# Kernel tuning notes

Measured on AMD Instinct MI355X. Metric: run time of the kernel, lower is better.

The kernel has to match this reference:

```python
import jax, jax.numpy as jnp
import numpy as np
from jax import lax

T = 16        # in_length
E = 32        # input_embedding_size_d
H = 64        # encoder_size
NG = 32       # vehicles per scene group
G = 1024      # number of scene groups
N = G * NG    # total vehicles
C = 3         # class_num

leaky = lambda x: jax.nn.leaky_relu(x, 0.1)

def _gru_final(x_seq, Wih, Whh, bih, bhh):
    # x_seq: (T, N, E). PyTorch GRU gate order: r, z, n. Returns final hidden (N, H).
    def step(h, x):
        gx = x @ Wih.T + bih
        gh = h @ Whh.T + bhh
        xr, xz, xn = jnp.split(gx, 3, axis=-1)
        hr, hz, hn = jnp.split(gh, 3, axis=-1)
        r = jax.nn.sigmoid(xr + hr)
        z = jax.nn.sigmoid(xz + hz)
        ng = jnp.tanh(xn + r * hn)
        return (1.0 - z) * ng + z * h, None
    h0 = jnp.zeros((x_seq.shape[1], Whh.shape[1]), x_seq.dtype)
    hT, _ = lax.scan(step, h0, x_seq)
    return hT

def setup_inputs() -> dict:
    key = jax.random.key(0)
    ks = jax.random.split(key, 24)
    def rn(k, shape, fan):
        return jax.random.normal(k, shape, jnp.float32) * np.float32(1.0 / np.sqrt(fan))
    inp = {}
    inp["scene"] = jax.random.normal(ks[0], (N, 2 * T), jnp.float32)
    inp["condition"] = jax.random.randint(ks[1], (N,), 0, C, jnp.int32)
    inp["hero_pos_index"] = jax.random.randint(ks[2], (G,), 0, N, jnp.int32)
    inp["nbrs_pos_index"] = jax.random.randint(ks[3], (N,), 0, N, jnp.int32)
    inp["index_div"] = jnp.arange(N, dtype=jnp.int32).reshape(G, NG)
    # ip_emb_d: Linear(2, E)
    inp["W_emb"] = rn(ks[4], (2, E), 2)
    inp["b_emb"] = jnp.zeros((E,), jnp.float32)
    # forward / backward GRUs (weight_ih: (3H,E), weight_hh: (3H,H))
    inp["Wih_f"] = rn(ks[5], (3 * H, E), E); inp["Whh_f"] = rn(ks[6], (3 * H, H), H)
    inp["bih_f"] = jnp.zeros((3 * H,), jnp.float32); inp["bhh_f"] = jnp.zeros((3 * H,), jnp.float32)
    inp["Wih_b"] = rn(ks[7], (3 * H, E), E); inp["Whh_b"] = rn(ks[8], (3 * H, H), H)
    inp["bih_b"] = jnp.zeros((3 * H,), jnp.float32); inp["bhh_b"] = jnp.zeros((3 * H,), jnp.float32)
    # mlp: Linear(H, H//2)
    inp["Wm"] = rn(ks[9], (H, H // 2), H); inp["bm"] = jnp.zeros((H // 2,), jnp.float32)
    # spatial_mlp: Linear(2T, H) -> Linear(H, H//2)
    inp["Ws1"] = rn(ks[10], (2 * T, H), 2 * T); inp["bs1"] = jnp.zeros((H,), jnp.float32)
    inp["Ws2"] = rn(ks[11], (H, H // 2), H); inp["bs2"] = jnp.zeros((H // 2,), jnp.float32)
    # op_d: Linear(H, H//4) -> Linear(H//4, C)
    inp["Wo1"] = rn(ks[12], (H, H // 4), H); inp["bo1"] = jnp.zeros((H // 4,), jnp.float32)
    inp["Wo2"] = rn(ks[13], (H // 4, C), H // 4); inp["bo2"] = jnp.zeros((C,), jnp.float32)
    return inp

def reference(scene, condition, hero_pos_index, nbrs_pos_index, index_div,
              W_emb, b_emb, Wih_f, Whh_f, bih_f, bhh_f, Wih_b, Whh_b, bih_b, bhh_b,
              Wm, bm, Ws1, bs1, Ws2, bs2, Wo1, bo1, Wo2, bo2):
    n_total = scene.shape[0]
    # scene.view(-1,2,T).permute(2,0,1) -> (T, N, 2)
    scene_t = scene.reshape(n_total, 2, T).transpose(2, 0, 1)
    emb = leaky(scene_t @ W_emb + b_emb)                 # (T, N, E)
    h_f = _gru_final(emb, Wih_f, Whh_f, bih_f, bhh_f)    # (N, H)
    h_b = _gru_final(emb[::-1], Wih_b, Whh_b, bih_b, bhh_b)
    seq_enc = leaky(((h_f + h_b) * 0.5) @ Wm + bm)       # (N, H//2)
    # pairwise relative features within each group: rel[g, j, i] = x_i - x_j
    feat_g = scene[index_div]                            # (G, n, 2T); row layout == permute(1,2,0).view(-1,2T)
    rel = feat_g[:, None, :, :] - feat_g[:, :, None, :]  # (G, n, n, 2T)
    enc = leaky(leaky(rel @ Ws1 + bs1) @ Ws2 + bs2)      # (G, n, n, H//2)
    # diagonal pairs (i==j) are dropped in the original; subtract mlp(0) then divide by n-1
    zero_enc = leaky(leaky(bs1) @ Ws2 + bs2)             # (H//2,)
    n_grp = index_div.shape[1]
    pooled = (enc.sum(axis=2) - zero_enc) / (n_grp - 1)  # (G, n, H//2)
    pooled = pooled.reshape(n_total, -1)                 # group-concat order == vehicle order (arange groups)
    full_enc = jnp.concatenate([seq_enc, pooled], axis=1)  # (N, H)
    x_logit = leaky(full_enc @ Wo1 + bo1) @ Wo2 + bo2      # (N, C)
    return x_logit, full_enc
```

## Files before the change

kernel.cpp:

```cpp
#include <hip/hip_runtime.h>
#include <hip/hip_bf16.h>

#define TT 16
#define EE 32
#define HH 64
#define NGRP 32
#define CC 3

typedef __attribute__((ext_vector_type(8))) short short8;
typedef __attribute__((ext_vector_type(4))) float floatx4;

#define MFMA16(a, b, c) __builtin_amdgcn_mfma_f32_16x16x32_bf16((a), (b), (c), 0, 0, 0)

__device__ __forceinline__ float leakyf(float x) { return fmaxf(x, 0.1f * x); }
__device__ __forceinline__ float sigmoidf_fast(float x) {
    return __builtin_amdgcn_rcpf(1.0f + __expf(-x));
}
__device__ __forceinline__ float tanhf_fast(float x) {
    return 1.0f - 2.0f * __builtin_amdgcn_rcpf(__expf(2.0f * x) + 1.0f);
}
__device__ __forceinline__ short f2bf(float x) {
    unsigned u = __float_as_uint(x);
    return (short)((u + 0x7FFFu + ((u >> 16) & 1u)) >> 16);
}
__device__ __forceinline__ short f2bf_h(float x) {
    return (short)((__float_as_uint(x) + 0x8000u) >> 16);
}
__device__ __forceinline__ float bf2f(short s) {
    return __uint_as_float(((unsigned)(unsigned short)s) << 16);
}
__device__ __forceinline__ short8 ld8bf(const float* __restrict__ p) {
    const float4 a = *(const float4*)p;
    const float4 b = *(const float4*)(p + 4);
    short8 v;
    v[0] = f2bf(a.x); v[1] = f2bf(a.y); v[2] = f2bf(a.z); v[3] = f2bf(a.w);
    v[4] = f2bf(b.x); v[5] = f2bf(b.y); v[6] = f2bf(b.z); v[7] = f2bf(b.w);
    return v;
}

__global__ __launch_bounds__(512, 4) void fused_kernel(
    const float* __restrict__ scene, const int* __restrict__ index_div,
    const float* __restrict__ W_emb, const float* __restrict__ b_emb,
    const float* __restrict__ Wih_f, const float* __restrict__ Whh_f,
    const float* __restrict__ bih_f, const float* __restrict__ bhh_f,
    const float* __restrict__ Wih_b, const float* __restrict__ Whh_b,
    const float* __restrict__ bih_b, const float* __restrict__ bhh_b,
    const float* __restrict__ Wm, const float* __restrict__ bm,
    const float* __restrict__ Ws1, const float* __restrict__ bs1,
    const float* __restrict__ Ws2, const float* __restrict__ bs2,
    const float* __restrict__ Wo1, const float* __restrict__ bo1,
    const float* __restrict__ Wo2, const float* __restrict__ bo2,
    float* __restrict__ full_enc, float* __restrict__ out)
{
    __shared__ float sscene[32][33];
    __shared__ __align__(16) union SmemU {
        struct {
            short Xall[16 * 2 * 64 * 8];
            short Hf[2 * 2 * 2 * 64 * 8];
        } g;
        struct {
            float su[NGRP][68];
            float fe[NGRP][68];
            float swo1[1024];
            float szero[32];
        } s;
    } sm;

    const int g    = blockIdx.x;
    const int tid  = threadIdx.x;
    const int lane = tid & 63;
    const int w    = __builtin_amdgcn_readfirstlane(tid >> 6);
    const int dir  = w >> 2;
    const int wd   = w & 3;
    const int cc   = lane & 15;
    const int quad = lane >> 4;
    const int j    = wd * 16 + cc;
    const int ks_w = j >> 5;
    const int qa_w = (j >> 3) & 3;
    const int ii_w = j & 7;

    #pragma unroll
    for (int rep = 0; rep < 2; ++rep) {
        const int idx = tid + rep * 512;
        const int v = idx >> 5, c = idx & 31;
        const int n = index_div[g * NGRP + v];
        sscene[c][v] = scene[n * 32 + c];
    }

    const float* Wih = dir ? Wih_b : Wih_f;
    const float* Whh = dir ? Whh_b : Whh_f;
    const float* bih = dir ? bih_b : bih_f;
    const float* bhh = dir ? bhh_b : bhh_f;
    const int k0 = quad * 8;
    const short8 Br0  = ld8bf(Whh + (j      ) * 64 + k0);
    const short8 Br1  = ld8bf(Whh + (j      ) * 64 + 32 + k0);
    const short8 Br2  = ld8bf(Wih + (j      ) * 32 + k0);
    const short8 Bz0  = ld8bf(Whh + (j +  64) * 64 + k0);
    const short8 Bz1  = ld8bf(Whh + (j +  64) * 64 + 32 + k0);
    const short8 Bz2  = ld8bf(Wih + (j +  64) * 32 + k0);
    const short8 Bhn0 = ld8bf(Whh + (j + 128) * 64 + k0);
    const short8 Bhn1 = ld8bf(Whh + (j + 128) * 64 + 32 + k0);
    const short8 Bxn  = ld8bf(Wih + (j + 128) * 32 + k0);
    const float b_r  = bih[j] + bhh[j];
    const float b_z  = bih[j + 64] + bhh[j + 64];
    const float b_xn = bih[j + 128];
    const float b_hn = bhh[j + 128];

    __syncthreads();

    {
        const int t   = tid >> 5;
        const int veh = tid & 31;
        const float xs = sscene[t][veh];
        const float ys = sscene[16 + t][veh];
        const int mt = veh >> 4;
        const int m  = veh & 15;
        #pragma unroll
        for (int q = 0; q < 4; ++q) {
            short8 v;
            #pragma unroll
            for (int i2 = 0; i2 < 8; ++i2) {
                const int e = q * 8 + i2;
                v[i2] = f2bf(leakyf(fmaf(xs, W_emb[e], fmaf(ys, W_emb[EE + e], b_emb[e]))));
            }
            *(short8*)&sm.g.Xall[(((t * 2 + mt) * 64) + q * 16 + m) * 8] = v;
        }
        const short8 z8 = {0, 0, 0, 0, 0, 0, 0, 0};
        *(short8*)&sm.g.Hf[tid * 8] = z8;
    }

    float h_reg[8];
    #pragma unroll
    for (int i = 0; i < 8; ++i) h_reg[i] = 0.0f;

    short* HfD = &sm.g.Hf[dir * (2 * 2 * 64 * 8)];
    __syncthreads();

    #pragma unroll 1
    for (int s = 0; s < TT; ++s) {
        const int t = dir ? (TT - 1 - s) : s;
        #pragma unroll
        for (int mt = 0; mt < 2; ++mt) {
            const short8 Ah0 = *(const short8*)&HfD[((0 * 2 + mt) * 64 + lane) * 8];
            const short8 Ah1 = *(const short8*)&HfD[((1 * 2 + mt) * 64 + lane) * 8];
            const short8 Axx = *(const short8*)&sm.g.Xall[((t * 2 + mt) * 64 + lane) * 8];
            const floatx4 z4 = {0.f, 0.f, 0.f, 0.f};
            const floatx4 ar  = MFMA16(Axx, Br2, MFMA16(Ah1, Br1, MFMA16(Ah0, Br0, z4)));
            const floatx4 az  = MFMA16(Axx, Bz2, MFMA16(Ah1, Bz1, MFMA16(Ah0, Bz0, z4)));
            const floatx4 ahn = MFMA16(Ah1, Bhn1, MFMA16(Ah0, Bhn0, z4));
            const floatx4 axn = MFMA16(Axx, Bxn, z4);
            #pragma unroll
            for (int r = 0; r < 4; ++r) {
                const float rr = sigmoidf_fast(ar[r] + b_r);
                const float zz = sigmoidf_fast(az[r] + b_z);
                const float ng = tanhf_fast(fmaf(rr, ahn[r] + b_hn, axn[r] + b_xn));
                const float h0 = h_reg[mt * 4 + r];
                h_reg[mt * 4 + r] = fmaf(zz, h0 - ng, ng);
            }
        }
        __syncthreads();
        #pragma unroll
        for (int mt = 0; mt < 2; ++mt) {
            #pragma unroll
            for (int r = 0; r < 4; ++r) {
                const int la = qa_w * 16 + (quad * 4 + r);
                HfD[((ks_w * 2 + mt) * 64 + la) * 8 + ii_w] = f2bf_h(h_reg[mt * 4 + r]);
            }
        }
        __syncthreads();
    }

    if (w < 4) {
        const int nt   = w >> 1;
        const int mt_e = w & 1;
        const int n_col = nt * 16 + cc;
        short8 Bm0, Bm1;
        #pragma unroll
        for (int i = 0; i < 8; ++i) {
            Bm0[i] = f2bf(Wm[(     quad * 8 + i) * 32 + n_col]);
            Bm1[i] = f2bf(Wm[(32 + quad * 8 + i) * 32 + n_col]);
        }
        short8 A0, A1;
        #pragma unroll
        for (int ks = 0; ks < 2; ++ks) {
            const short8 F = *(const short8*)&sm.g.Hf[0 * 2048 + ((ks * 2 + mt_e) * 64 + lane) * 8];
            const short8 B = *(const short8*)&sm.g.Hf[1 * 2048 + ((ks * 2 + mt_e) * 64 + lane) * 8];
            #pragma unroll
            for (int i = 0; i < 8; ++i) {
                const short v = f2bf(0.5f * (bf2f(F[i]) + bf2f(B[i])));
                if (ks == 0) A0[i] = v; else A1[i] = v;
            }
        }
        const floatx4 z4 = {0.f, 0.f, 0.f, 0.f};
        const floatx4 acc = MFMA16(A1, Bm1, MFMA16(A0, Bm0, z4));
        const float bmn = bm[n_col];
        #pragma unroll
        for (int r = 0; r < 4; ++r) {
            const int veh = mt_e * 16 + quad * 4 + r;
            const float sv = leakyf(acc[r] + bmn);
            const int n = index_div[g * NGRP + veh];
            full_enc[n * HH + n_col] = sv;
            sm.s.fe[veh][n_col] = sv;
        }
    } else {
        const int l  = tid & 255;
        const int v  = l >> 3;
        const int d0 = (l & 7) * 8;
        float acc[8];
        #pragma unroll
        for (int i = 0; i < 8; ++i) acc[i] = 0.0f;
        #pragma unroll
        for (int e = 0; e < EE; ++e) {
            const float f = sscene[e][v];
            const float4 w0 = *(const float4*)&Ws1[e * 64 + d0];
            const float4 w1 = *(const float4*)&Ws1[e * 64 + d0 + 4];
            acc[0] = fmaf(f, w0.x, acc[0]); acc[1] = fmaf(f, w0.y, acc[1]);
            acc[2] = fmaf(f, w0.z, acc[2]); acc[3] = fmaf(f, w0.w, acc[3]);
            acc[4] = fmaf(f, w1.x, acc[4]); acc[5] = fmaf(f, w1.y, acc[5]);
            acc[6] = fmaf(f, w1.z, acc[6]); acc[7] = fmaf(f, w1.w, acc[7]);
        }
        #pragma unroll
        for (int i = 0; i < 8; ++i) sm.s.su[v][d0 + i] = acc[i];
        *(float4*)&sm.s.swo1[l * 4] = *(const float4*)&Wo1[l * 4];
        if (l < 32) {
            float zs = bs2[l];
            #pragma unroll
            for (int d = 0; d < HH; ++d) zs = fmaf(leakyf(bs1[d]), Ws2[d * 32 + l], zs);
            sm.s.szero[l] = leakyf(zs);
        }
    }

    short8 Bw00, Bw01, Bw10, Bw11;
    #pragma unroll
    for (int i = 0; i < 8; ++i) {
        Bw00[i] = f2bf(Ws2[(     quad * 8 + i) * 32 + cc]);
        Bw01[i] = f2bf(Ws2[(32 + quad * 8 + i) * 32 + cc]);
        Bw10[i] = f2bf(Ws2[(     quad * 8 + i) * 32 + 16 + cc]);
        Bw11[i] = f2bf(Ws2[(32 + quad * 8 + i) * 32 + 16 + cc]);
    }
    float bsq0[8], bsq1[8];
    #pragma unroll
    for (int i = 0; i < 8; ++i) {
        bsq0[i] = bs1[quad * 8 + i];
        bsq1[i] = bs1[32 + quad * 8 + i];
    }
    const float bs2c0 = bs2[cc], bs2c1 = bs2[16 + cc];
    __syncthreads();

    #pragma unroll 2
    for (int jj = 0; jj < 4; ++jj) {
        const int jrow = w * 4 + jj;
        float vj0[8], vj1[8];
        #pragma unroll
        for (int i = 0; i < 8; ++i) {
            vj0[i] = sm.s.su[jrow][quad * 8 + i] - bsq0[i];
            vj1[i] = sm.s.su[jrow][32 + quad * 8 + i] - bsq1[i];
        }
        float acc0 = 0.0f, acc1 = 0.0f;
        #pragma unroll
        for (int it = 0; it < 2; ++it) {
            const int irow = it * 16 + cc;
            const float4 p0 = *(const float4*)&sm.s.su[irow][quad * 8];
            const float4 p1 = *(const float4*)&sm.s.su[irow][quad * 8 + 4];
            const float4 p2 = *(const float4*)&sm.s.su[irow][32 + quad * 8];
            const float4 p3 = *(const float4*)&sm.s.su[irow][32 + quad * 8 + 4];
            short8 A0, A1;
            A0[0] = f2bf(leakyf(p0.x - vj0[0])); A0[1] = f2bf(leakyf(p0.y - vj0[1]));
            A0[2] = f2bf(leakyf(p0.z - vj0[2])); A0[3] = f2bf(leakyf(p0.w - vj0[3]));
            A0[4] = f2bf(leakyf(p1.x - vj0[4])); A0[5] = f2bf(leakyf(p1.y - vj0[5]));
            A0[6] = f2bf(leakyf(p1.z - vj0[6])); A0[7] = f2bf(leakyf(p1.w - vj0[7]));
            A1[0] = f2bf(leakyf(p2.x - vj1[0])); A1[1] = f2bf(leakyf(p2.y - vj1[1]));
            A1[2] = f2bf(leakyf(p2.z - vj1[2])); A1[3] = f2bf(leakyf(p2.w - vj1[3]));
            A1[4] = f2bf(leakyf(p3.x - vj1[4])); A1[5] = f2bf(leakyf(p3.y - vj1[5]));
            A1[6] = f2bf(leakyf(p3.z - vj1[6])); A1[7] = f2bf(leakyf(p3.w - vj1[7]));
            const floatx4 z4 = {0.f, 0.f, 0.f, 0.f};
            const floatx4 D0 = MFMA16(A1, Bw01, MFMA16(A0, Bw00, z4));
            const floatx4 D1 = MFMA16(A1, Bw11, MFMA16(A0, Bw10, z4));
            #pragma unroll
            for (int r = 0; r < 4; ++r) {
                acc0 += leakyf(D0[r] + bs2c0);
                acc1 += leakyf(D1[r] + bs2c1);
            }
        }
        acc0 += __shfl_xor(acc0, 16, 64); acc0 += __shfl_xor(acc0, 32, 64);
        acc1 += __shfl_xor(acc1, 16, 64); acc1 += __shfl_xor(acc1, 32, 64);
        const int n = index_div[g * NGRP + jrow];
        if (quad == 0) {
            const float pv = (acc0 - sm.s.szero[cc]) * (1.0f / 31.0f);
            full_enc[n * HH + 32 + cc] = pv;
            sm.s.fe[jrow][32 + cc] = pv;
        } else if (quad == 1) {
            const float pv = (acc1 - sm.s.szero[16 + cc]) * (1.0f / 31.0f);
            full_enc[n * HH + 48 + cc] = pv;
            sm.s.fe[jrow][48 + cc] = pv;
        }
    }
    __syncthreads();

    {
        const int veh = tid >> 4;
        const int p   = tid & 15;
        float a = bo1[p];
        #pragma unroll
        for (int k = 0; k < HH; ++k)
            a = fmaf(sm.s.fe[veh][k], sm.s.swo1[k * 16 + p], a);
        a = leakyf(a);
        float l0 = a * Wo2[p * 3 + 0];
        float l1 = a * Wo2[p * 3 + 1];
        float l2 = a * Wo2[p * 3 + 2];
        #pragma unroll
        for (int off = 1; off < 16; off <<= 1) {
            l0 += __shfl_xor(l0, off, 64);
            l1 += __shfl_xor(l1, off, 64);
            l2 += __shfl_xor(l2, off, 64);
        }
        if (p == 0) {
            const int n = index_div[g * NGRP + veh];
            out[n * 3 + 0] = l0 + bo2[0];
            out[n * 3 + 1] = l1 + bo2[1];
            out[n * 3 + 2] = l2 + bo2[2];
        }
    }
}

extern "C" void kernel_launch(void* const* d_in, const int* in_sizes, int n_in,
                              void* d_out, int out_size, void* d_ws, size_t ws_size,
                              hipStream_t stream) {
    const float* scene     = (const float*)d_in[0];
    const int*   index_div = (const int*)d_in[4];
    const float* W_emb = (const float*)d_in[5];
    const float* b_emb = (const float*)d_in[6];
    const float* Wih_f = (const float*)d_in[7];
    const float* Whh_f = (const float*)d_in[8];
    const float* bih_f = (const float*)d_in[9];
    const float* bhh_f = (const float*)d_in[10];
    const float* Wih_b = (const float*)d_in[11];
    const float* Whh_b = (const float*)d_in[12];
    const float* bih_b = (const float*)d_in[13];
    const float* bhh_b = (const float*)d_in[14];
    const float* Wm  = (const float*)d_in[15];
    const float* bm  = (const float*)d_in[16];
    const float* Ws1 = (const float*)d_in[17];
    const float* bs1 = (const float*)d_in[18];
    const float* Ws2 = (const float*)d_in[19];
    const float* bs2 = (const float*)d_in[20];
    const float* Wo1 = (const float*)d_in[21];
    const float* bo1 = (const float*)d_in[22];
    const float* Wo2 = (const float*)d_in[23];
    const float* bo2 = (const float*)d_in[24];

    const int N = in_sizes[0] / (2 * TT);
    const int G = in_sizes[4] / NGRP;

    float* out      = (float*)d_out;
    float* full_enc = out + (size_t)N * CC;

    fused_kernel<<<dim3(G), dim3(512), 0, stream>>>(
        scene, index_div, W_emb, b_emb, Wih_f, Whh_f, bih_f, bhh_f,
        Wih_b, Whh_b, bih_b, bhh_b, Wm, bm, Ws1, bs1, Ws2, bs2,
        Wo1, bo1, Wo2, bo2, full_enc, out);
}
```

Measured before the change: 194.7 us.

## Double-buffer GRU hidden state, fold activation scales into weights, raise occupancy

Double-buffers the shared-memory hidden state so each GRU step needs only one barrier instead of two. Pre-scales the gate weights and biases by -1/ln2 and 2/ln2, feeds the biases in as the MFMA accumulator init, and uses exp2 directly, which removes per-element multiplies and adds from the recurrence. Permutes the hidden-state write slots and read lanes to reduce LDS bank conflicts, and raises the launch-bounds occupancy hint from 4 to 6. In exchange it doubles the Hf buffer, puts more pressure on registers, and rounds the scaled weights to bf16, which changes precision slightly.

```diff
diff --git a/kernel.cpp b/kernel.cpp
--- a/kernel.cpp
+++ b/kernel.cpp
@@ -12,13 +12,9 @@
 
 #define MFMA16(a, b, c) __builtin_amdgcn_mfma_f32_16x16x32_bf16((a), (b), (c), 0, 0, 0)
 
+#define RLN2 1.4426950408889634f
+
 __device__ __forceinline__ float leakyf(float x) { return fmaxf(x, 0.1f * x); }
-__device__ __forceinline__ float sigmoidf_fast(float x) {
-    return __builtin_amdgcn_rcpf(1.0f + __expf(-x));
-}
-__device__ __forceinline__ float tanhf_fast(float x) {
-    return 1.0f - 2.0f * __builtin_amdgcn_rcpf(__expf(2.0f * x) + 1.0f);
-}
 __device__ __forceinline__ short f2bf(float x) {
     unsigned u = __float_as_uint(x);
     return (short)((u + 0x7FFFu + ((u >> 16) & 1u)) >> 16);
@@ -37,8 +33,16 @@
     v[4] = f2bf(b.x); v[5] = f2bf(b.y); v[6] = f2bf(b.z); v[7] = f2bf(b.w);
     return v;
 }
-
-__global__ __launch_bounds__(512, 4) void fused_kernel(
+__device__ __forceinline__ short8 ld8bfs(const float* __restrict__ p, float s) {
+    const float4 a = *(const float4*)p;
+    const float4 b = *(const float4*)(p + 4);
+    short8 v;
+    v[0] = f2bf(a.x * s); v[1] = f2bf(a.y * s); v[2] = f2bf(a.z * s); v[3] = f2bf(a.w * s);
+    v[4] = f2bf(b.x * s); v[5] = f2bf(b.y * s); v[6] = f2bf(b.z * s); v[7] = f2bf(b.w * s);
+    return v;
+}
+
+__global__ __launch_bounds__(512, 6) void fused_kernel(
     const float* __restrict__ scene, const int* __restrict__ index_div,
     const float* __restrict__ W_emb, const float* __restrict__ b_emb,
     const float* __restrict__ Wih_f, const float* __restrict__ Whh_f,
@@ -56,7 +60,7 @@
     __shared__ __align__(16) union SmemU {
         struct {
             short Xall[16 * 2 * 64 * 8];
-            short Hf[2 * 2 * 2 * 64 * 8];
+            short Hf[2 * 2 * 2 * 2 * 64 * 8];
         } g;
         struct {
             float su[NGRP][68];
@@ -78,6 +82,7 @@
     const int ks_w = j >> 5;
     const int qa_w = (j >> 3) & 3;
     const int ii_w = j & 7;
+    const int rlane = (lane & 48) | ((lane & 3) << 2) | ((lane >> 2) & 3);
 
     #pragma unroll
     for (int rep = 0; rep < 2; ++rep) {
@@ -92,19 +97,24 @@
     const float* bih = dir ? bih_b : bih_f;
     const float* bhh = dir ? bhh_b : bhh_f;
     const int k0 = quad * 8;
-    const short8 Br0  = ld8bf(Whh + (j      ) * 64 + k0);
-    const short8 Br1  = ld8bf(Whh + (j      ) * 64 + 32 + k0);
-    const short8 Br2  = ld8bf(Wih + (j      ) * 32 + k0);
-    const short8 Bz0  = ld8bf(Whh + (j +  64) * 64 + k0);
-    const short8 Bz1  = ld8bf(Whh + (j +  64) * 64 + 32 + k0);
-    const short8 Bz2  = ld8bf(Wih + (j +  64) * 32 + k0);
-    const short8 Bhn0 = ld8bf(Whh + (j + 128) * 64 + k0);
-    const short8 Bhn1 = ld8bf(Whh + (j + 128) * 64 + 32 + k0);
-    const short8 Bxn  = ld8bf(Wih + (j + 128) * 32 + k0);
-    const float b_r  = bih[j] + bhh[j];
-    const float b_z  = bih[j + 64] + bhh[j + 64];
-    const float b_xn = bih[j + 128];
-    const float b_hn = bhh[j + 128];
+    const float SRZ = -RLN2, SN = 2.0f * RLN2;
+    const short8 Br0  = ld8bfs(Whh + (j      ) * 64 + k0,      SRZ);
+    const short8 Br1  = ld8bfs(Whh + (j      ) * 64 + 32 + k0, SRZ);
+    const short8 Br2  = ld8bfs(Wih + (j      ) * 32 + k0,      SRZ);
+    const short8 Bz0  = ld8bfs(Whh + (j +  64) * 64 + k0,      SRZ);
+    const short8 Bz1  = ld8bfs(Whh + (j +  64) * 64 + 32 + k0, SRZ);
+    const short8 Bz2  = ld8bfs(Wih + (j +  64) * 32 + k0,      SRZ);
+    const short8 Bhn0 = ld8bfs(Whh + (j + 128) * 64 + k0,      SN);
+    const short8 Bhn1 = ld8bfs(Whh + (j + 128) * 64 + 32 + k0, SN);
+    const short8 Bxn  = ld8bfs(Wih + (j + 128) * 32 + k0,      SN);
+    const float vb_r  = SRZ * (bih[j] + bhh[j]);
+    const float vb_z  = SRZ * (bih[j + 64] + bhh[j + 64]);
+    const float vb_xn = SN * bih[j + 128];
+    const float vb_hn = SN * bhh[j + 128];
+    const floatx4 c_r  = {vb_r,  vb_r,  vb_r,  vb_r };
+    const floatx4 c_z  = {vb_z,  vb_z,  vb_z,  vb_z };
+    const floatx4 c_xn = {vb_xn, vb_xn, vb_xn, vb_xn};
+    const floatx4 c_hn = {vb_hn, vb_hn, vb_hn, vb_hn};
 
     __syncthreads();
 
@@ -126,45 +136,49 @@
             *(short8*)&sm.g.Xall[(((t * 2 + mt) * 64) + q * 16 + m) * 8] = v;
         }
         const short8 z8 = {0, 0, 0, 0, 0, 0, 0, 0};
-        *(short8*)&sm.g.Hf[tid * 8] = z8;
+        *(short8*)&sm.g.Hf[(tid >> 8) * 4096 + (tid & 255) * 8] = z8;
     }
 
     float h_reg[8];
     #pragma unroll
     for (int i = 0; i < 8; ++i) h_reg[i] = 0.0f;
 
-    short* HfD = &sm.g.Hf[dir * (2 * 2 * 64 * 8)];
+    const int hf_dir = dir * 4096;
     __syncthreads();
 
-    #pragma unroll 1
+    #pragma unroll 2
     for (int s = 0; s < TT; ++s) {
-        const int t = dir ? (TT - 1 - s) : s;
+        const int pb = s & 1, nb = pb ^ 1;
+        const int t  = dir ? (TT - 1 - s) : s;
+        const short* HfD = &sm.g.Hf[hf_dir + pb * 2048];
+        short*       HfN = &sm.g.Hf[hf_dir + nb * 2048];
         #pragma unroll
         for (int mt = 0; mt < 2; ++mt) {
-            const short8 Ah0 = *(const short8*)&HfD[((0 * 2 + mt) * 64 + lane) * 8];
-            const short8 Ah1 = *(const short8*)&HfD[((1 * 2 + mt) * 64 + lane) * 8];
+            const short8 Ah0 = *(const short8*)&HfD[((0 * 2 + mt) * 64 + rlane) * 8];
+            const short8 Ah1 = *(const short8*)&HfD[((1 * 2 + mt) * 64 + rlane) * 8];
             const short8 Axx = *(const short8*)&sm.g.Xall[((t * 2 + mt) * 64 + lane) * 8];
-            const floatx4 z4 = {0.f, 0.f, 0.f, 0.f};
-            const floatx4 ar  = MFMA16(Axx, Br2, MFMA16(Ah1, Br1, MFMA16(Ah0, Br0, z4)));
-            const floatx4 az  = MFMA16(Axx, Bz2, MFMA16(Ah1, Bz1, MFMA16(Ah0, Bz0, z4)));
-            const floatx4 ahn = MFMA16(Ah1, Bhn1, MFMA16(Ah0, Bhn0, z4));
-            const floatx4 axn = MFMA16(Axx, Bxn, z4);
+            const floatx4 ar  = MFMA16(Axx, Br2, MFMA16(Ah1, Br1, MFMA16(Ah0, Br0, c_r)));
+            const floatx4 az  = MFMA16(Axx, Bz2, MFMA16(Ah1, Bz1, MFMA16(Ah0, Bz0, c_z)));
+            const floatx4 ahn = MFMA16(Ah1, Bhn1, MFMA16(Ah0, Bhn0, c_hn));
+            const floatx4 axn = MFMA16(Axx, Bxn, c_xn);
             #pragma unroll
             for (int r = 0; r < 4; ++r) {
-                const float rr = sigmoidf_fast(ar[r] + b_r);
-                const float zz = sigmoidf_fast(az[r] + b_z);
-                const float ng = tanhf_fast(fmaf(rr, ahn[r] + b_hn, axn[r] + b_xn));
+                const float rr = __builtin_amdgcn_rcpf(1.0f + __builtin_amdgcn_exp2f(ar[r]));
+                const float zz = __builtin_amdgcn_rcpf(1.0f + __builtin_amdgcn_exp2f(az[r]));
+                const float y  = fmaf(rr, ahn[r], axn[r]);
+                const float ng = fmaf(-2.0f,
+                                      __builtin_amdgcn_rcpf(__builtin_amdgcn_exp2f(y) + 1.0f),
+                                      1.0f);
                 const float h0 = h_reg[mt * 4 + r];
                 h_reg[mt * 4 + r] = fmaf(zz, h0 - ng, ng);
             }
         }
-        __syncthreads();
         #pragma unroll
         for (int mt = 0; mt < 2; ++mt) {
             #pragma unroll
             for (int r = 0; r < 4; ++r) {
-                const int la = qa_w * 16 + (quad * 4 + r);
-                HfD[((ks_w * 2 + mt) * 64 + la) * 8 + ii_w] = f2bf_h(h_reg[mt * 4 + r]);
+                const int slot = qa_w * 16 + r * 4 + quad;
+                HfN[((ks_w * 2 + mt) * 64 + slot) * 8 + ii_w] = f2bf_h(h_reg[mt * 4 + r]);
             }
         }
         __syncthreads();
@@ -183,8 +197,8 @@
         short8 A0, A1;
         #pragma unroll
         for (int ks = 0; ks < 2; ++ks) {
-            const short8 F = *(const short8*)&sm.g.Hf[0 * 2048 + ((ks * 2 + mt_e) * 64 + lane) * 8];
-            const short8 B = *(const short8*)&sm.g.Hf[1 * 2048 + ((ks * 2 + mt_e) * 64 + lane) * 8];
+            const short8 F = *(const short8*)&sm.g.Hf[0    + ((ks * 2 + mt_e) * 64 + rlane) * 8];
+            const short8 B = *(const short8*)&sm.g.Hf[4096 + ((ks * 2 + mt_e) * 64 + rlane) * 8];
             #pragma unroll
             for (int i = 0; i < 8; ++i) {
                 const short v = f2bf(0.5f * (bf2f(F[i]) + bf2f(B[i])));
```

Result: slower. 417.4 us (+114.4%).
